# Kernel tuning notes

Hardware: AMD Instinct MI355X
Metric: run time of the kernel (lower is better)

## Reference

```python
import jax, jax.numpy as jnp
import numpy as np

NUM_HEADS = 16
MASKED_BIAS = -10000.0


def setup_inputs() -> dict:
    key = jax.random.key(0)
    k1, k2, k3 = jax.random.split(key, 3)
    B, S, D = 4, 2048, 1024
    scale = 0.02
    return {
        "hidden_states": jax.random.normal(k1, (B, S, D), dtype=jnp.float32),
        "c_attn_w": jax.random.normal(k2, (D, 3 * D), dtype=jnp.float32) * scale,
        "c_attn_b": jnp.zeros((3 * D,), dtype=jnp.float32),
        "c_proj_w": jax.random.normal(k3, (D, D), dtype=jnp.float32) * scale,
        "c_proj_b": jnp.zeros((D,), dtype=jnp.float32),
    }


def reference(hidden_states, c_attn_w, c_attn_b, c_proj_w, c_proj_b):
    B, S, D = hidden_states.shape
    H = NUM_HEADS
    hd = D // H
    # qkv projection (HF Conv1D: x @ W + b)
    qkv = hidden_states @ c_attn_w + c_attn_b  # [B, S, 3D]
    q, k, v = jnp.split(qkv, 3, axis=-1)

    def split_heads(t):
        return t.reshape(B, S, H, hd).transpose(0, 2, 1, 3)  # [B, H, S, hd]

    q, k, v = split_heads(q), split_heads(k), split_heads(v)
    # full score matrix [B, H, S, S] (eager attention)
    attn = jnp.einsum("bhqd,bhkd->bhqk", q, k) / jnp.sqrt(jnp.float32(hd))
    causal = jnp.tril(jnp.ones((S, S), dtype=bool))  # [S, S]
    attn = jnp.where(causal[None, None], attn, jnp.float32(MASKED_BIAS))
    attn = jax.nn.softmax(attn, axis=-1)
    out = jnp.einsum("bhqk,bhkd->bhqd", attn, v)  # [B, H, S, hd]
    out = out.transpose(0, 2, 1, 3).reshape(B, S, D)  # merge heads
    out = out @ c_proj_w + c_proj_b
    return out
```

## Files before the change

### kernel.cpp

```cpp
#include <hip/hip_runtime.h>

#define NH 16
#define HD 64

typedef __attribute__((ext_vector_type(8))) _Float16 f16x8;
typedef __attribute__((ext_vector_type(4))) float f32x4;
typedef __attribute__((ext_vector_type(16))) float f32x16;
typedef __attribute__((ext_vector_type(8))) unsigned short us8;
typedef __attribute__((ext_vector_type(4))) unsigned short us4;
typedef __attribute__((ext_vector_type(2))) unsigned int u32x2;

#define CEXP 0.18033688f

__device__ __forceinline__ unsigned short f2h(float f) {
    _Float16 h = (_Float16)f;
    return __builtin_bit_cast(unsigned short, h);
}

__global__ __launch_bounds__(256)
void transpose_cast_both(const float* __restrict__ w1, unsigned short* __restrict__ o1,
                         const float* __restrict__ w2, unsigned short* __restrict__ o2) {
    __shared__ float T[64][65];
    const int R = 1024;
    int bx = blockIdx.x;
    const float* in; unsigned short* out; int C;
    if (bx < 48) { in = w1; out = o1; C = 3072; }
    else         { in = w2; out = o2; C = 1024; bx -= 48; }
    const int c0 = bx * 64, r0 = blockIdx.y * 64;
    const int tid = threadIdx.x;
    const int rr = tid >> 4, cc4 = (tid & 15) * 4;
    #pragma unroll
    for (int p = 0; p < 4; ++p) {
        int r = rr + p * 16;
        float4 v = *reinterpret_cast<const float4*>(
            in + (size_t)(r0 + r) * C + c0 + cc4);
        T[r][cc4] = v.x; T[r][cc4 + 1] = v.y; T[r][cc4 + 2] = v.z; T[r][cc4 + 3] = v.w;
    }
    __syncthreads();
    #pragma unroll
    for (int p = 0; p < 4; ++p) {
        int orow = rr + p * 16;
        us4 w;
        #pragma unroll
        for (int j = 0; j < 4; ++j) w[j] = f2h(T[cc4 + j][orow]);
        *reinterpret_cast<us4*>(out + (size_t)(c0 + orow) * R + r0 + cc4) = w;
    }
}

__device__ __forceinline__ void stage128(unsigned short* dst,
                                         const unsigned short* src, int stride) {
    const int tid = threadIdx.x;
    #pragma unroll
    for (int p = 0; p < 4; ++p) {
        int idx = tid + p * 256;
        int r = idx >> 3;
        int slot = idx & 7;
        us8 v = *reinterpret_cast<const us8*>(src + (size_t)r * stride + slot * 8);
        int cb = (slot << 4) ^ ((r & 7) << 4);
        *reinterpret_cast<us8*>(reinterpret_cast<char*>(dst) + r * 128 + cb) = v;
    }
}

__device__ __forceinline__ void stage128_f32(unsigned short* dst,
                                             const float* src, int stride) {
    const int tid = threadIdx.x;
    #pragma unroll
    for (int p = 0; p < 4; ++p) {
        int idx = tid + p * 256;
        int r = idx >> 3;
        int slot = idx & 7;
        const float* s = src + (size_t)r * stride + slot * 8;
        float4 a = *reinterpret_cast<const float4*>(s);
        float4 b = *reinterpret_cast<const float4*>(s + 4);
        uint4 w;
        w.x = __builtin_bit_cast(unsigned int, __builtin_amdgcn_cvt_pkrtz(a.x, a.y));
        w.y = __builtin_bit_cast(unsigned int, __builtin_amdgcn_cvt_pkrtz(a.z, a.w));
        w.z = __builtin_bit_cast(unsigned int, __builtin_amdgcn_cvt_pkrtz(b.x, b.y));
        w.w = __builtin_bit_cast(unsigned int, __builtin_amdgcn_cvt_pkrtz(b.z, b.w));
        int cb = (slot << 4) ^ ((r & 7) << 4);
        *reinterpret_cast<uint4*>(reinterpret_cast<char*>(dst) + r * 128 + cb) = w;
    }
}

__device__ __forceinline__ void stage64(unsigned short* dst,
                                        const unsigned short* src, int stride) {
    const int tid = threadIdx.x;
    #pragma unroll
    for (int p = 0; p < 2; ++p) {
        int idx = tid + p * 256;
        int r = idx >> 3;
        int slot = idx & 7;
        us8 v = *reinterpret_cast<const us8*>(src + (size_t)r * stride + slot * 8);
        int cb = (slot << 4) ^ ((r & 7) << 4);
        *reinterpret_cast<us8*>(reinterpret_cast<char*>(dst) + r * 128 + cb) = v;
    }
}

__device__ __forceinline__ f16x8 frag16(const unsigned short* base, int row0, int ks) {
    const int lane = threadIdx.x & 63;
    const int r = row0 + (lane & 15);
    int cb = ((ks << 6) + (lane & 48)) ^ ((r & 7) << 4);
    return *reinterpret_cast<const f16x8*>(
        reinterpret_cast<const char*>(base) + r * 128 + cb);
}

__device__ __forceinline__ f16x8 frag32(const unsigned short* base, int row0, int c) {
    const int lane = threadIdx.x & 63;
    const int r = row0 + (lane & 31);
    int cb = ((c << 5) + ((lane >> 5) << 4)) ^ ((r & 7) << 4);
    return *reinterpret_cast<const f16x8*>(
        reinterpret_cast<const char*>(base) + r * 128 + cb);
}

template<int MODE, int NX>
__global__ __launch_bounds__(256)
void gemm_f16(const void* __restrict__ Ax,
              const unsigned short* __restrict__ Bt,
              const float* __restrict__ bias,
              float* __restrict__ C,
              unsigned short* __restrict__ qb,
              unsigned short* __restrict__ kb,
              unsigned short* __restrict__ vtb,
              int M, int N, int K) {
    __shared__ __align__(16) unsigned short As[128 * 64];
    __shared__ __align__(16) unsigned short Bs[128 * 64];

    const int tid = threadIdx.x;
    const int wid = tid >> 6, lane = tid & 63, g = lane >> 4;
    const int wr = wid >> 1, wc = wid & 1;

    const int f = blockIdx.x;
    const int wi = f >> 3;
    const int m0 = ((wi / NX) * 8 + (f & 7)) * 128;
    const int n0 = (wi % NX) * 128;

    f32x4 acc[4][4];
    #pragma unroll
    for (int i = 0; i < 4; ++i)
        #pragma unroll
        for (int j = 0; j < 4; ++j) {
            acc[i][j][0] = 0.f; acc[i][j][1] = 0.f;
            acc[i][j][2] = 0.f; acc[i][j][3] = 0.f;
        }

    for (int k0 = 0; k0 < K; k0 += 64) {
        __syncthreads();
        if (MODE == 1)
            stage128_f32(As, (const float*)Ax + (size_t)m0 * K + k0, K);
        else
            stage128(As, (const unsigned short*)Ax + (size_t)m0 * K + k0, K);
        stage128(Bs, Bt + (size_t)n0 * K + k0, K);
        __syncthreads();

        f16x8 af[4][2], bf[4][2];
        #pragma unroll
        for (int mi = 0; mi < 4; ++mi)
            #pragma unroll
            for (int ks = 0; ks < 2; ++ks)
                af[mi][ks] = frag16(As, wr * 64 + mi * 16, ks);
        #pragma unroll
        for (int ni = 0; ni < 4; ++ni)
            #pragma unroll
            for (int ks = 0; ks < 2; ++ks)
                bf[ni][ks] = frag16(Bs, wc * 64 + ni * 16, ks);

        __builtin_amdgcn_s_setprio(1);
        #pragma unroll
        for (int ks = 0; ks < 2; ++ks)
            #pragma unroll
            for (int mi = 0; mi < 4; ++mi)
                #pragma unroll
                for (int ni = 0; ni < 4; ++ni)
                    acc[mi][ni] = __builtin_amdgcn_mfma_f32_16x16x32_f16(
                        af[mi][ks], bf[ni][ks], acc[mi][ni], 0, 0, 0);
        __builtin_amdgcn_s_setprio(0);
    }

    const int colBase = n0 + wc * 64;
    const int rowBase = m0 + wr * 64;

    if (MODE == 0) {
        #pragma unroll
        for (int ni = 0; ni < 4; ++ni) {
            int col = colBase + ni * 16 + (lane & 15);
            float bv = bias[col];
            #pragma unroll
            for (int mi = 0; mi < 4; ++mi) {
                int row = rowBase + mi * 16 + g * 4;
                #pragma unroll
                for (int reg = 0; reg < 4; ++reg)
                    C[(size_t)(row + reg) * N + col] = acc[mi][ni][reg] + bv;
            }
        }
    } else {
        #pragma unroll
        for (int ni = 0; ni < 4; ++ni) {
            int col = colBase + ni * 16 + (lane & 15);
            float bv = bias[col];
            int seg = col >> 10;
            int cc = col & 1023;
            int h = cc >> 6, d = cc & 63;
            const float sc = (seg == 0) ? CEXP : 1.0f;
            #pragma unroll
            for (int mi = 0; mi < 4; ++mi) {
                int row = rowBase + mi * 16 + g * 4;
                int b = row >> 11, s = row & 2047;
                size_t bh = (size_t)(b * NH + h);
                if (seg < 2) {
                    unsigned short* dst = (seg ? kb : qb)
                        + bh * 2048 * 64 + (size_t)s * 64 + d;
                    #pragma unroll
                    for (int reg = 0; reg < 4; ++reg)
                        dst[(size_t)reg * 64] = f2h((acc[mi][ni][reg] + bv) * sc);
                } else {
                    unsigned short* dst = vtb
                        + bh * 64 * 2048 + (size_t)d * 2048 + s;
                    us4 w;
                    #pragma unroll
                    for (int reg = 0; reg < 4; ++reg)
                        w[reg] = f2h(acc[mi][ni][reg] + bv);
                    *reinterpret_cast<us4*>(dst) = w;
                }
            }
        }
    }
}

template<bool DIAG>
__device__ __forceinline__ void attn_slice(
    const f16x8 (&qf)[4],
    const unsigned short* Ks, const unsigned short* Vs, unsigned short* Pw,
    f32x16 (&o)[2], float& l_, int kt, int qsb, int lane) {

    const int hf = lane >> 5;
    const int q = lane & 31;

    f32x16 s[2];
    #pragma unroll
    for (int n = 0; n < 2; ++n)
        #pragma unroll
        for (int r = 0; r < 16; ++r) s[n][r] = 0.f;

    __builtin_amdgcn_s_setprio(1);
    #pragma unroll
    for (int c = 0; c < 4; ++c) {
        #pragma unroll
        for (int n = 0; n < 2; ++n)
            s[n] = __builtin_amdgcn_mfma_f32_32x32x16_f16(
                frag32(Ks, n * 32, c), qf[c], s[n], 0, 0, 0);
    }
    __builtin_amdgcn_s_setprio(0);

    const int qg = qsb + q;
    float psum = 0.f;
    #pragma unroll
    for (int n = 0; n < 2; ++n) {
        #pragma unroll
        for (int j = 0; j < 4; ++j) {
            float p[4];
            #pragma unroll
            for (int i = 0; i < 4; ++i) {
                float v = __builtin_exp2f(s[n][j * 4 + i]);
                if (DIAG) {
                    int kg = kt * 64 + n * 32 + 8 * j + 4 * hf + i;
                    if (kg > qg) v = 0.f;
                }
                p[i] = v; psum += v;
            }
            u32x2 w;
            w[0] = __builtin_bit_cast(unsigned int, __builtin_amdgcn_cvt_pkrtz(p[0], p[1]));
            w[1] = __builtin_bit_cast(unsigned int, __builtin_amdgcn_cvt_pkrtz(p[2], p[3]));
            int pb = (n * 64 + j * 16 + hf * 8) ^ ((q & 7) << 4);
            *reinterpret_cast<u32x2*>(
                reinterpret_cast<char*>(Pw) + q * 128 + pb) = w;
        }
    }
    l_ += psum;

    __builtin_amdgcn_s_setprio(1);
    #pragma unroll
    for (int c = 0; c < 4; ++c) {
        f16x8 pf = frag32(Pw, 0, c);
        #pragma unroll
        for (int n2 = 0; n2 < 2; ++n2)
            o[n2] = __builtin_amdgcn_mfma_f32_32x32x16_f16(
                pf, frag32(Vs, n2 * 32, c), o[n2], 0, 0, 0);
    }
    __builtin_amdgcn_s_setprio(0);
}

__global__ __launch_bounds__(256, 2)
void attn_mfma(const unsigned short* __restrict__ qb,
               const unsigned short* __restrict__ kb,
               const unsigned short* __restrict__ vtb,
               unsigned short* __restrict__ attno) {
    const int f = blockIdx.x;
    const int xcd = f & 7;
    const int wi = f >> 3;
    const int bh = xcd * 8 + (wi >> 3);
    const int t = wi & 7;
    const int cA = t, cB = 15 - t;
    const int tid = threadIdx.x;
    const int wid = tid >> 6, lane = tid & 63;

    __shared__ __align__(16) unsigned short Ks[64 * 64];
    __shared__ __align__(16) unsigned short Vs[64 * 64];
    __shared__ __align__(16) unsigned short Ps[4][32 * 64];

    const unsigned short* kg0 = kb + (size_t)bh * 2048 * 64;
    const unsigned short* vg0 = vtb + (size_t)bh * 64 * 2048;

    const int qsbA = cA * 128 + wid * 32;
    const int qsbB = cB * 128 + wid * 32;
    const int mA = qsbA >> 6, mB = qsbB >> 6;

    const unsigned short* qbase = qb + (size_t)bh * 2048 * 64;
    const int qoff = ((lane >> 5) << 4);
    f16x8 qfA[4], qfB[4];
    #pragma unroll
    for (int c = 0; c < 4; ++c) {
        qfA[c] = *reinterpret_cast<const f16x8*>(
            reinterpret_cast<const char*>(qbase + (size_t)(qsbA + (lane & 31)) * 64)
            + c * 32 + qoff);
        qfB[c] = *reinterpret_cast<const f16x8*>(
            reinterpret_cast<const char*>(qbase + (size_t)(qsbB + (lane & 31)) * 64)
            + c * 32 + qoff);
    }

    f32x16 oA[2], oB[2];
    #pragma unroll
    for (int n = 0; n < 2; ++n)
        #pragma unroll
        for (int r = 0; r < 16; ++r) { oA[n][r] = 0.f; oB[n][r] = 0.f; }
    float lA = 0.f, lB = 0.f;

    unsigned short* Pw = Ps[wid];
    const int kmax = 2 * cB + 1;

    for (int kt = 0; kt <= kmax; ++kt) {
        __syncthreads();
        stage64(Ks, kg0 + (size_t)kt * 64 * 64, 64);
        stage64(Vs, vg0 + (size_t)kt * 64, 2048);
        __syncthreads();

        if (kt < mB)       attn_slice<false>(qfB, Ks, Vs, Pw, oB, lB, kt, qsbB, lane);
        else if (kt == mB) attn_slice<true >(qfB, Ks, Vs, Pw, oB, lB, kt, qsbB, lane);
        if (kt < mA)       attn_slice<false>(qfA, Ks, Vs, Pw, oA, lA, kt, qsbA, lane);
        else if (kt == mA) attn_slice<true >(qfA, Ks, Vs, Pw, oA, lA, kt, qsbA, lane);
    }

    const int b = bh >> 4, hh = bh & 15;
    const int hf = lane >> 5;
    #pragma unroll
    for (int ph = 0; ph < 2; ++ph) {
        const int qsb = ph ? qsbB : qsbA;
        f32x16* o = ph ? oB : oA;
        float ltot = ph ? lB : lA;
        ltot += __shfl_xor(ltot, 32);
        unsigned short* ob = attno
            + (size_t)(b * 2048 + qsb) * 1024 + hh * 64 + (lane & 31);
        #pragma unroll
        for (int n2 = 0; n2 < 2; ++n2) {
            #pragma unroll
            for (int j = 0; j < 4; ++j)
                #pragma unroll
                for (int i = 0; i < 4; ++i) {
                    int qloc = i + 8 * j + 4 * hf;
                    float inv = 1.0f / __shfl(ltot, qloc);
                    ob[(size_t)qloc * 1024 + n2 * 32] = f2h(o[n2][j * 4 + i] * inv);
                }
        }
    }
}

extern "C" void kernel_launch(void* const* d_in, const int* in_sizes, int n_in,
                              void* d_out, int out_size, void* d_ws, size_t ws_size,
                              hipStream_t stream) {
    const float* x    = (const float*)d_in[0];
    const float* Wqkv = (const float*)d_in[1];
    const float* bqkv = (const float*)d_in[2];
    const float* Wp   = (const float*)d_in[3];
    const float* bp   = (const float*)d_in[4];
    float* out = (float*)d_out;

    const int B = 4, S = 2048, D = 1024;
    const int M = B * S;
    const size_t HSZ = (size_t)M * D;

    unsigned short* wqt   = (unsigned short*)d_ws;
    unsigned short* wpt   = wqt + (size_t)3 * D * D;
    unsigned short* qbuf  = wpt + (size_t)D * D;
    unsigned short* kbuf  = qbuf + HSZ;
    unsigned short* vtb   = kbuf + HSZ;
    unsigned short* attno = vtb + HSZ;

    dim3 blk(256);
    transpose_cast_both<<<dim3(64, 16), blk, 0, stream>>>(Wqkv, wqt, Wp, wpt);

    gemm_f16<1, 24><<<dim3(1536), blk, 0, stream>>>(
        x, wqt, bqkv, nullptr, qbuf, kbuf, vtb, M, 3 * D, D);
    attn_mfma<<<dim3(512), blk, 0, stream>>>(qbuf, kbuf, vtb, attno);
    gemm_f16<0, 8><<<dim3(512), blk, 0, stream>>>(
        attno, wpt, bp, out, nullptr, nullptr, nullptr, M, D, D);
}
```

Measured before the change: 174.8 us.

## Double-buffer GEMM tiles with direct global-to-LDS loads and pre-cast input

```diff
diff --git a/kernel.cpp b/kernel.cpp
--- a/kernel.cpp
+++ b/kernel.cpp
@@ -15,6 +15,19 @@
 __device__ __forceinline__ unsigned short f2h(float f) {
     _Float16 h = (_Float16)f;
     return __builtin_bit_cast(unsigned short, h);
+}
+
+#define GL16(gp, lp) __builtin_amdgcn_global_load_lds(                        \
+    (const __attribute__((address_space(1))) void*)(gp),                      \
+    (__attribute__((address_space(3))) void*)(lp), 16, 0, 0)
+
+__global__ __launch_bounds__(256)
+void cast_f16(const float* __restrict__ in, unsigned short* __restrict__ out) {
+    size_t i = ((size_t)blockIdx.x * 256 + threadIdx.x) * 4;
+    float4 v = *reinterpret_cast<const float4*>(in + i);
+    us4 w;
+    w[0] = f2h(v.x); w[1] = f2h(v.y); w[2] = f2h(v.z); w[3] = f2h(v.w);
+    *reinterpret_cast<us4*>(out + i) = w;
 }
 
 __global__ __launch_bounds__(256)
@@ -47,41 +60,6 @@
     }
 }
 
-__device__ __forceinline__ void stage128(unsigned short* dst,
-                                         const unsigned short* src, int stride) {
-    const int tid = threadIdx.x;
-    #pragma unroll
-    for (int p = 0; p < 4; ++p) {
-        int idx = tid + p * 256;
-        int r = idx >> 3;
-        int slot = idx & 7;
-        us8 v = *reinterpret_cast<const us8*>(src + (size_t)r * stride + slot * 8);
-        int cb = (slot << 4) ^ ((r & 7) << 4);
-        *reinterpret_cast<us8*>(reinterpret_cast<char*>(dst) + r * 128 + cb) = v;
-    }
-}
-
-__device__ __forceinline__ void stage128_f32(unsigned short* dst,
-                                             const float* src, int stride) {
-    const int tid = threadIdx.x;
-    #pragma unroll
-    for (int p = 0; p < 4; ++p) {
-        int idx = tid + p * 256;
-        int r = idx >> 3;
-        int slot = idx & 7;
-        const float* s = src + (size_t)r * stride + slot * 8;
-        float4 a = *reinterpret_cast<const float4*>(s);
-        float4 b = *reinterpret_cast<const float4*>(s + 4);
-        uint4 w;
-        w.x = __builtin_bit_cast(unsigned int, __builtin_amdgcn_cvt_pkrtz(a.x, a.y));
-        w.y = __builtin_bit_cast(unsigned int, __builtin_amdgcn_cvt_pkrtz(a.z, a.w));
-        w.z = __builtin_bit_cast(unsigned int, __builtin_amdgcn_cvt_pkrtz(b.x, b.y));
-        w.w = __builtin_bit_cast(unsigned int, __builtin_amdgcn_cvt_pkrtz(b.z, b.w));
-        int cb = (slot << 4) ^ ((r & 7) << 4);
-        *reinterpret_cast<uint4*>(reinterpret_cast<char*>(dst) + r * 128 + cb) = w;
-    }
-}
-
 __device__ __forceinline__ void stage64(unsigned short* dst,
                                         const unsigned short* src, int stride) {
     const int tid = threadIdx.x;
@@ -96,6 +74,20 @@
     }
 }
 
+__device__ __forceinline__ void stage128_gl(unsigned short* dst,
+                                            const unsigned short* src,
+                                            int strideElems, int wid, int lane) {
+    const char* s = (const char*)src;
+    #pragma unroll
+    for (int i = 0; i < 4; ++i) {
+        int rbase = wid * 32 + i * 8;
+        int row = rbase + (lane >> 3);
+        int slot = (lane & 7) ^ (row & 7);
+        GL16(s + (size_t)row * (2 * strideElems) + slot * 16,
+             (char*)dst + rbase * 128);
+    }
+}
+
 __device__ __forceinline__ f16x8 frag16(const unsigned short* base, int row0, int ks) {
     const int lane = threadIdx.x & 63;
     const int r = row0 + (lane & 15);
@@ -114,7 +106,7 @@
 
 template<int MODE, int NX>
 __global__ __launch_bounds__(256)
-void gemm_f16(const void* __restrict__ Ax,
+void gemm_f16(const unsigned short* __restrict__ A,
               const unsigned short* __restrict__ Bt,
               const float* __restrict__ bias,
               float* __restrict__ C,
@@ -122,8 +114,8 @@
               unsigned short* __restrict__ kb,
               unsigned short* __restrict__ vtb,
               int M, int N, int K) {
-    __shared__ __align__(16) unsigned short As[128 * 64];
-    __shared__ __align__(16) unsigned short Bs[128 * 64];
+    __shared__ __align__(16) unsigned short As[2][128 * 64];
+    __shared__ __align__(16) unsigned short Bs[2][128 * 64];
 
     const int tid = threadIdx.x;
     const int wid = tid >> 6, lane = tid & 63, g = lane >> 4;
@@ -134,6 +126,9 @@
     const int m0 = ((wi / NX) * 8 + (f & 7)) * 128;
     const int n0 = (wi % NX) * 128;
 
+    const unsigned short* Ab = A + (size_t)m0 * K;
+    const unsigned short* Bb = Bt + (size_t)n0 * K;
+
     f32x4 acc[4][4];
     #pragma unroll
     for (int i = 0; i < 4; ++i)
@@ -143,26 +138,30 @@
             acc[i][j][2] = 0.f; acc[i][j][3] = 0.f;
         }
 
+    stage128_gl(As[0], Ab, K, wid, lane);
+    stage128_gl(Bs[0], Bb, K, wid, lane);
+
+    int cur = 0;
     for (int k0 = 0; k0 < K; k0 += 64) {
         __syncthreads();
-        if (MODE == 1)
-            stage128_f32(As, (const float*)Ax + (size_t)m0 * K + k0, K);
-        else
-            stage128(As, (const unsigned short*)Ax + (size_t)m0 * K + k0, K);
-        stage128(Bs, Bt + (size_t)n0 * K + k0, K);
-        __syncthreads();
-
+        if (k0 + 64 < K) {
+            stage128_gl(As[cur ^ 1], Ab + k0 + 64, K, wid, lane);
+            stage128_gl(Bs[cur ^ 1], Bb + k0 + 64, K, wid, lane);
+        }
+
+        const unsigned short* Ac = As[cur];
+        const unsigned short* Bc = Bs[cur];
         f16x8 af[4][2], bf[4][2];
         #pragma unroll
         for (int mi = 0; mi < 4; ++mi)
             #pragma unroll
             for (int ks = 0; ks < 2; ++ks)
-                af[mi][ks] = frag16(As, wr * 64 + mi * 16, ks);
+                af[mi][ks] = frag16(Ac, wr * 64 + mi * 16, ks);
         #pragma unroll
         for (int ni = 0; ni < 4; ++ni)
             #pragma unroll
             for (int ks = 0; ks < 2; ++ks)
-                bf[ni][ks] = frag16(Bs, wc * 64 + ni * 16, ks);
+                bf[ni][ks] = frag16(Bc, wc * 64 + ni * 16, ks);
 
         __builtin_amdgcn_s_setprio(1);
         #pragma unroll
@@ -174,6 +173,7 @@
                     acc[mi][ni] = __builtin_amdgcn_mfma_f32_16x16x32_f16(
                         af[mi][ks], bf[ni][ks], acc[mi][ni], 0, 0, 0);
         __builtin_amdgcn_s_setprio(0);
+        cur ^= 1;
     }
 
     const int colBase = n0 + wc * 64;
@@ -387,7 +387,8 @@
     const int M = B * S;
     const size_t HSZ = (size_t)M * D;
 
-    unsigned short* wqt   = (unsigned short*)d_ws;
+    unsigned short* xh    = (unsigned short*)d_ws;
+    unsigned short* wqt   = xh + HSZ;
     unsigned short* wpt   = wqt + (size_t)3 * D * D;
     unsigned short* qbuf  = wpt + (size_t)D * D;
     unsigned short* kbuf  = qbuf + HSZ;
@@ -395,10 +396,11 @@
     unsigned short* attno = vtb + HSZ;
 
     dim3 blk(256);
+    cast_f16<<<dim3((int)(HSZ / 1024)), blk, 0, stream>>>(x, xh);
     transpose_cast_both<<<dim3(64, 16), blk, 0, stream>>>(Wqkv, wqt, Wp, wpt);
 
     gemm_f16<1, 24><<<dim3(1536), blk, 0, stream>>>(
-        x, wqt, bqkv, nullptr, qbuf, kbuf, vtb, M, 3 * D, D);
+        xh, wqt, bqkv, nullptr, qbuf, kbuf, vtb, M, 3 * D, D);
     attn_mfma<<<dim3(512), blk, 0, stream>>>(qbuf, kbuf, vtb, attno);
     gemm_f16<0, 8><<<dim3(512), blk, 0, stream>>>(
         attno, wpt, bp, out, nullptr, nullptr, nullptr, M, D, D);
```

Result: slower. 181.1 us (+3.6%).

## Double-buffer GEMM LDS tiles with direct global-to-LDS loads

Applied to the files above, without the earlier changes.

```diff
diff --git a/kernel.cpp b/kernel.cpp
--- a/kernel.cpp
+++ b/kernel.cpp
@@ -16,6 +16,10 @@
     _Float16 h = (_Float16)f;
     return __builtin_bit_cast(unsigned short, h);
 }
+
+#define GL16(gp, lp) __builtin_amdgcn_global_load_lds(                        \
+    (const __attribute__((address_space(1))) void*)(gp),                      \
+    (__attribute__((address_space(3))) void*)(lp), 16, 0, 0)
 
 __global__ __launch_bounds__(256)
 void transpose_cast_both(const float* __restrict__ w1, unsigned short* __restrict__ o1,
@@ -47,11 +51,11 @@
     }
 }
 
-__device__ __forceinline__ void stage128(unsigned short* dst,
-                                         const unsigned short* src, int stride) {
+__device__ __forceinline__ void stage64(unsigned short* dst,
+                                        const unsigned short* src, int stride) {
     const int tid = threadIdx.x;
     #pragma unroll
-    for (int p = 0; p < 4; ++p) {
+    for (int p = 0; p < 2; ++p) {
         int idx = tid + p * 256;
         int r = idx >> 3;
         int slot = idx & 7;
@@ -82,17 +86,17 @@
     }
 }
 
-__device__ __forceinline__ void stage64(unsigned short* dst,
-                                        const unsigned short* src, int stride) {
-    const int tid = threadIdx.x;
-    #pragma unroll
-    for (int p = 0; p < 2; ++p) {
-        int idx = tid + p * 256;
-        int r = idx >> 3;
-        int slot = idx & 7;
-        us8 v = *reinterpret_cast<const us8*>(src + (size_t)r * stride + slot * 8);
-        int cb = (slot << 4) ^ ((r & 7) << 4);
-        *reinterpret_cast<us8*>(reinterpret_cast<char*>(dst) + r * 128 + cb) = v;
+__device__ __forceinline__ void stage128_gl(unsigned short* dst,
+                                            const unsigned short* src,
+                                            int strideElems, int wid, int lane) {
+    const char* s = (const char*)src;
+    #pragma unroll
+    for (int i = 0; i < 4; ++i) {
+        int rbase = wid * 32 + i * 8;
+        int row = rbase + (lane >> 3);
+        int slot = (lane & 7) ^ (row & 7);
+        GL16(s + (size_t)row * (2 * strideElems) + slot * 16,
+             (char*)dst + rbase * 128);
     }
 }
 
@@ -122,8 +126,10 @@
               unsigned short* __restrict__ kb,
               unsigned short* __restrict__ vtb,
               int M, int N, int K) {
-    __shared__ __align__(16) unsigned short As[128 * 64];
-    __shared__ __align__(16) unsigned short Bs[128 * 64];
+    __shared__ __align__(16) unsigned short As0[128 * 64];
+    __shared__ __align__(16) unsigned short As1[128 * 64];
+    __shared__ __align__(16) unsigned short Bs0[128 * 64];
+    __shared__ __align__(16) unsigned short Bs1[128 * 64];
 
     const int tid = threadIdx.x;
     const int wid = tid >> 6, lane = tid & 63, g = lane >> 4;
@@ -134,6 +140,8 @@
     const int m0 = ((wi / NX) * 8 + (f & 7)) * 128;
     const int n0 = (wi % NX) * 128;
 
+    const unsigned short* Bb = Bt + (size_t)n0 * K;
+
     f32x4 acc[4][4];
     #pragma unroll
     for (int i = 0; i < 4; ++i)
@@ -143,38 +151,60 @@
             acc[i][j][2] = 0.f; acc[i][j][3] = 0.f;
         }
 
-    for (int k0 = 0; k0 < K; k0 += 64) {
+#define STAGE_A(buf, koff)                                                    \
+    do {                                                                      \
+        if (MODE == 1)                                                        \
+            stage128_f32(buf, (const float*)Ax + (size_t)m0 * K + (koff), K); \
+        else                                                                  \
+            stage128_gl(buf, (const unsigned short*)Ax + (size_t)m0 * K +     \
+                        (koff), K, wid, lane);                                \
+    } while (0)
+
+#define GEMM_COMPUTE(Abuf, Bbuf)                                              \
+    do {                                                                      \
+        f16x8 af[4][2], bf[4][2];                                             \
+        _Pragma("unroll")                                                     \
+        for (int mi = 0; mi < 4; ++mi)                                        \
+            _Pragma("unroll")                                                 \
+            for (int ks = 0; ks < 2; ++ks)                                    \
+                af[mi][ks] = frag16(Abuf, wr * 64 + mi * 16, ks);             \
+        _Pragma("unroll")                                                     \
+        for (int ni = 0; ni < 4; ++ni)                                        \
+            _Pragma("unroll")                                                 \
+            for (int ks = 0; ks < 2; ++ks)                                    \
+                bf[ni][ks] = frag16(Bbuf, wc * 64 + ni * 16, ks);             \
+        __builtin_amdgcn_s_setprio(1);                                        \
+        _Pragma("unroll")                                                     \
+        for (int ks = 0; ks < 2; ++ks)                                        \
+            _Pragma("unroll")                                                 \
+            for (int mi = 0; mi < 4; ++mi)                                    \
+                _Pragma("unroll")                                             \
+                for (int ni = 0; ni < 4; ++ni)                                \
+                    acc[mi][ni] = __builtin_amdgcn_mfma_f32_16x16x32_f16(     \
+                        af[mi][ks], bf[ni][ks], acc[mi][ni], 0, 0, 0);        \
+        __builtin_amdgcn_s_setprio(0);                                        \
+    } while (0)
+
+    STAGE_A(As0, 0);
+    stage128_gl(Bs0, Bb, K, wid, lane);
+
+    #pragma unroll 1
+    for (int k0 = 0; k0 < K; k0 += 128) {
         __syncthreads();
-        if (MODE == 1)
-            stage128_f32(As, (const float*)Ax + (size_t)m0 * K + k0, K);
-        else
-            stage128(As, (const unsigned short*)Ax + (size_t)m0 * K + k0, K);
-        stage128(Bs, Bt + (size_t)n0 * K + k0, K);
+        if (k0 + 64 < K) {
+            stage128_gl(Bs1, Bb + k0 + 64, K, wid, lane);
+            STAGE_A(As1, k0 + 64);
+        }
+        GEMM_COMPUTE(As0, Bs0);
         __syncthreads();
-
-        f16x8 af[4][2], bf[4][2];
-        #pragma unroll
-        for (int mi = 0; mi < 4; ++mi)
-            #pragma unroll
-            for (int ks = 0; ks < 2; ++ks)
-                af[mi][ks] = frag16(As, wr * 64 + mi * 16, ks);
-        #pragma unroll
-        for (int ni = 0; ni < 4; ++ni)
-            #pragma unroll
-            for (int ks = 0; ks < 2; ++ks)
-                bf[ni][ks] = frag16(Bs, wc * 64 + ni * 16, ks);
-
-        __builtin_amdgcn_s_setprio(1);
-        #pragma unroll
-        for (int ks = 0; ks < 2; ++ks)
-            #pragma unroll
-            for (int mi = 0; mi < 4; ++mi)
-                #pragma unroll
-                for (int ni = 0; ni < 4; ++ni)
-                    acc[mi][ni] = __builtin_amdgcn_mfma_f32_16x16x32_f16(
-                        af[mi][ks], bf[ni][ks], acc[mi][ni], 0, 0, 0);
-        __builtin_amdgcn_s_setprio(0);
-    }
+        if (k0 + 128 < K) {
+            stage128_gl(Bs0, Bb + k0 + 128, K, wid, lane);
+            STAGE_A(As0, k0 + 128);
+        }
+        GEMM_COMPUTE(As1, Bs1);
+    }
+#undef STAGE_A
+#undef GEMM_COMPUTE
 
     const int colBase = n0 + wc * 64;
     const int rowBase = m0 + wr * 64;
```

Measured after the change: 176.0 us. Within noise of the previous version (+0.7%).
